# Performance work log

Measured on AMD Instinct MI355X. Metric: run time of the kernel, lower is better.

Reference implementation:

```python
import jax, jax.numpy as jnp
import numpy as np

B = 16          # graphs in batch
N = 10000       # original-graph nodes per graph
EG = 20000      # line-graph nodes (edges) per graph
E = B * EG      # total line-graph nodes
D = 384         # dim_inner
H = D // 3      # hdim
TOTAL_NODES = B * N


def setup_inputs() -> dict:
    key = jax.random.key(0)
    k1, k2 = jax.random.split(key)
    x = jax.random.normal(k1, (E, D), dtype=jnp.float32)
    org_graph_size = jnp.full((B,), N, dtype=jnp.int32)
    ptr = jnp.arange(B + 1, dtype=jnp.int32) * EG
    lg_node_idx = jax.random.randint(k2, (E, 2), 0, N, dtype=jnp.int32)
    return {"x": x, "org_graph_size": org_graph_size, "ptr": ptr, "lg_node_idx": lg_node_idx}


def _scatter_mean(x, idx, num_segments):
    # segment mean: sum / count (count clamped to 1 for empty segments)
    s = jax.ops.segment_sum(x, idx, num_segments=num_segments)
    c = jax.ops.segment_sum(jnp.ones((x.shape[0],), x.dtype), idx, num_segments=num_segments)
    return s / jnp.maximum(c, 1.0)[:, None]


def reference(x, org_graph_size, ptr, lg_node_idx):
    # per-graph node-index offsets (cumsum with leading zero, drop last)
    offsets = jnp.cumsum(
        jnp.concatenate([jnp.zeros((1,), org_graph_size.dtype), org_graph_size])
    )[:-1]
    # repeat each graph's offset for each of its line-graph nodes
    edge_counts = ptr[1:] - ptr[:-1]
    padding = jnp.repeat(offsets, edge_counts, total_repeat_length=E)
    idx = lg_node_idx + padding[:, None]  # [E, 2] global node indices

    outgoing = _scatter_mean(x, idx[:, 0], TOTAL_NODES)
    incoming = _scatter_mean(x, idx[:, 1], TOTAL_NODES)

    # lgvariant == 21
    return jnp.concatenate([incoming[:, : 2 * H], outgoing[:, 2 * H :]], axis=1)
```

## Files before the change

kernel.cpp:

```cpp
#include <hip/hip_runtime.h>

#define DIM 384
#define C4PER 96

#define SCAN_BLOCK 256
#define SCAN_ITEMS 8
#define SCAN_CHUNK (SCAN_BLOCK * SCAN_ITEMS)

__global__ void count_kernel(const int* __restrict__ org, const int* __restrict__ ptr,
                             const int2* __restrict__ lg2, int B, int E, int TN,
                             int* __restrict__ cnt, int2* __restrict__ rk) {
    int e = blockIdx.x * blockDim.x + threadIdx.x;
    if (e >= E) return;
    int off = 0;
    for (int j = 0; j < B; ++j)
        if (e >= ptr[j + 1]) off += org[j];
    int2 nn = lg2[e];
    int n_out = nn.x + off;
    int n_in  = nn.y + off;
    int r_in  = atomicAdd(&cnt[n_in], 1);
    int r_out = atomicAdd(&cnt[TN + n_out], 1);
    rk[e] = make_int2(r_out, r_in);
}

__global__ void scan1_kernel(const int* __restrict__ cnt, int* __restrict__ offs,
                             int* __restrict__ bsum, int n) {
    __shared__ int s[SCAN_BLOCK];
    int base = blockIdx.x * SCAN_CHUNK;
    int tid = threadIdx.x;
    int v[SCAN_ITEMS];
    int tsum = 0;
#pragma unroll
    for (int j = 0; j < SCAN_ITEMS; ++j) {
        int i = base + tid * SCAN_ITEMS + j;
        v[j] = (i < n) ? cnt[i] : 0;
        tsum += v[j];
    }
    s[tid] = tsum;
    __syncthreads();
    for (int d = 1; d < SCAN_BLOCK; d <<= 1) {
        int t = (tid >= d) ? s[tid - d] : 0;
        __syncthreads();
        s[tid] += t;
        __syncthreads();
    }
    if (tid == SCAN_BLOCK - 1) bsum[blockIdx.x] = s[SCAN_BLOCK - 1];
    int run = (tid > 0) ? s[tid - 1] : 0;
#pragma unroll
    for (int j = 0; j < SCAN_ITEMS; ++j) {
        int i = base + tid * SCAN_ITEMS + j;
        if (i < n) offs[i] = run;
        run += v[j];
    }
}

__global__ void scan2_kernel(int* __restrict__ bsum, int nb) {
    __shared__ int s[SCAN_BLOCK];
    int tid = threadIdx.x;
    int carry = 0;
    for (int base = 0; base < nb; base += SCAN_BLOCK) {
        int i = base + tid;
        s[tid] = (i < nb) ? bsum[i] : 0;
        __syncthreads();
        for (int d = 1; d < SCAN_BLOCK; d <<= 1) {
            int t = (tid >= d) ? s[tid - d] : 0;
            __syncthreads();
            s[tid] += t;
            __syncthreads();
        }
        int excl = carry + ((tid > 0) ? s[tid - 1] : 0);
        if (i < nb) bsum[i] = excl;
        carry += s[SCAN_BLOCK - 1];
        __syncthreads();
    }
}

__global__ void scan3_kernel(int* __restrict__ offs, const int* __restrict__ bsum, int n) {
    int i = blockIdx.x * blockDim.x + threadIdx.x;
    if (i < n) offs[i] += bsum[i / SCAN_CHUNK];
}

__global__ void fill_kernel(const int* __restrict__ org, const int* __restrict__ ptr,
                            const int2* __restrict__ lg2, const int2* __restrict__ rk,
                            const int* __restrict__ offs, int B, int E, int TN,
                            int* __restrict__ list) {
    int e = blockIdx.x * blockDim.x + threadIdx.x;
    if (e >= E) return;
    int off = 0;
    for (int j = 0; j < B; ++j)
        if (e >= ptr[j + 1]) off += org[j];
    int2 nn = lg2[e];
    int2 r  = rk[e];
    list[offs[nn.y + off] + r.y] = e;
    list[offs[TN + nn.x + off] + r.x] = e;
}

__global__ __launch_bounds__(256, 8)
void gather_kernel(const float4* __restrict__ x4,
                   const int* __restrict__ cnt, const int* __restrict__ offs,
                   const int* __restrict__ list,
                   float4* __restrict__ out4, int TN) {
    int i = blockIdx.x * blockDim.x + threadIdx.x;
    int tn64 = TN << 6;
    int node, c4, slot;
    if (i < tn64) {
        node = i >> 6;
        c4 = i & 63;
        slot = node;
    } else {
        int j = i - tn64;
        if (j >= (TN << 5)) return;
        node = j >> 5;
        c4 = 64 + (j & 31);
        slot = TN + node;
    }
    int start = offs[slot];
    int deg = cnt[slot];
    int end = start + deg;
    float4 acc = make_float4(0.f, 0.f, 0.f, 0.f);
    int k = start;
    for (; k + 1 < end; k += 2) {
        int e0 = list[k];
        int e1 = list[k + 1];
        float4 v0 = x4[e0 * C4PER + c4];
        float4 v1 = x4[e1 * C4PER + c4];
        acc.x += v0.x + v1.x;
        acc.y += v0.y + v1.y;
        acc.z += v0.z + v1.z;
        acc.w += v0.w + v1.w;
    }
    if (k < end) {
        int e0 = list[k];
        float4 v0 = x4[e0 * C4PER + c4];
        acc.x += v0.x; acc.y += v0.y; acc.z += v0.z; acc.w += v0.w;
    }
    float inv = 1.0f / (float)max(deg, 1);
    acc.x *= inv; acc.y *= inv; acc.z *= inv; acc.w *= inv;
    out4[node * C4PER + c4] = acc;
}

extern "C" void kernel_launch(void* const* d_in, const int* in_sizes, int n_in,
                              void* d_out, int out_size, void* d_ws, size_t ws_size,
                              hipStream_t stream) {
    const float* x = (const float*)d_in[0];
    const int* org = (const int*)d_in[1];
    const int* ptr = (const int*)d_in[2];
    const int* lg  = (const int*)d_in[3];

    int B  = in_sizes[1];
    int E  = in_sizes[3] / 2;
    int TN = out_size / DIM;
    int n2 = 2 * TN;

    int* cnt  = (int*)d_ws;
    int* offs = cnt + n2;
    int* bsum = offs + n2;
    int* list = bsum + 1024;
    int2* rk  = (int2*)(list + 2 * E);

    hipMemsetAsync(cnt, 0, (size_t)n2 * sizeof(int), stream);

    count_kernel<<<(E + 255) / 256, 256, 0, stream>>>(org, ptr, (const int2*)lg, B, E, TN,
                                                      cnt, rk);

    int nb = (n2 + SCAN_CHUNK - 1) / SCAN_CHUNK;
    scan1_kernel<<<nb, SCAN_BLOCK, 0, stream>>>(cnt, offs, bsum, n2);
    scan2_kernel<<<1, SCAN_BLOCK, 0, stream>>>(bsum, nb);
    scan3_kernel<<<(n2 + 255) / 256, 256, 0, stream>>>(offs, bsum, n2);

    fill_kernel<<<(E + 255) / 256, 256, 0, stream>>>(org, ptr, (const int2*)lg, rk, offs,
                                                     B, E, TN, list);

    int total = TN * C4PER;
    gather_kernel<<<(total + 255) / 256, 256, 0, stream>>>((const float4*)x, cnt, offs, list,
                                                           (float4*)d_out, TN);
}
```

Before: 759.8 us.

## Fold scan fixup into consumers, pack offset/count pairs, shuffle-broadcast edge lists

Removes the scan3 pass by having fill and gather add the block prefix (bsum[slot>>11]) on the fly. The local offset is stored together with the count as an int2, so each consumer does one load instead of two. In the gather, each lane of a wavefront (or half-wavefront) loads one list entry, and the entries are broadcast with __shfl, with a 4-way unrolled accumulation replacing serial list loads. Also adds size_t indexing and unroll pragmas, at the cost of extra shuffles and an extra bsum lookup per segment.

```diff
diff --git a/kernel.cpp b/kernel.cpp
--- a/kernel.cpp
+++ b/kernel.cpp
@@ -13,17 +13,16 @@
     int e = blockIdx.x * blockDim.x + threadIdx.x;
     if (e >= E) return;
     int off = 0;
+#pragma unroll 8
     for (int j = 0; j < B; ++j)
         if (e >= ptr[j + 1]) off += org[j];
     int2 nn = lg2[e];
-    int n_out = nn.x + off;
-    int n_in  = nn.y + off;
-    int r_in  = atomicAdd(&cnt[n_in], 1);
-    int r_out = atomicAdd(&cnt[TN + n_out], 1);
+    int r_in  = atomicAdd(&cnt[nn.y + off], 1);
+    int r_out = atomicAdd(&cnt[TN + nn.x + off], 1);
     rk[e] = make_int2(r_out, r_in);
 }
 
-__global__ void scan1_kernel(const int* __restrict__ cnt, int* __restrict__ offs,
+__global__ void scan1_kernel(const int* __restrict__ cnt, int2* __restrict__ pair,
                              int* __restrict__ bsum, int n) {
     __shared__ int s[SCAN_BLOCK];
     int base = blockIdx.x * SCAN_CHUNK;
@@ -49,7 +48,7 @@
 #pragma unroll
     for (int j = 0; j < SCAN_ITEMS; ++j) {
         int i = base + tid * SCAN_ITEMS + j;
-        if (i < n) offs[i] = run;
+        if (i < n) pair[i] = make_int2(run, v[j]);
         run += v[j];
     }
 }
@@ -75,68 +74,91 @@
     }
 }
 
-__global__ void scan3_kernel(int* __restrict__ offs, const int* __restrict__ bsum, int n) {
-    int i = blockIdx.x * blockDim.x + threadIdx.x;
-    if (i < n) offs[i] += bsum[i / SCAN_CHUNK];
-}
-
 __global__ void fill_kernel(const int* __restrict__ org, const int* __restrict__ ptr,
                             const int2* __restrict__ lg2, const int2* __restrict__ rk,
-                            const int* __restrict__ offs, int B, int E, int TN,
-                            int* __restrict__ list) {
+                            const int2* __restrict__ pair, const int* __restrict__ bsum,
+                            int B, int E, int TN, int* __restrict__ list) {
     int e = blockIdx.x * blockDim.x + threadIdx.x;
     if (e >= E) return;
     int off = 0;
+#pragma unroll 8
     for (int j = 0; j < B; ++j)
         if (e >= ptr[j + 1]) off += org[j];
     int2 nn = lg2[e];
     int2 r  = rk[e];
-    list[offs[nn.y + off] + r.y] = e;
-    list[offs[TN + nn.x + off] + r.x] = e;
+    int s_in  = nn.y + off;
+    int s_out = TN + nn.x + off;
+    list[pair[s_in].x  + bsum[s_in  >> 11] + r.y] = e;
+    list[pair[s_out].x + bsum[s_out >> 11] + r.x] = e;
+}
+
+template <int W>
+__device__ inline float4 gather_seg(const float4* __restrict__ x4,
+                                    const int* __restrict__ list,
+                                    int start, int deg, int c4, int sub) {
+    int e_l = (sub < deg) ? list[start + sub] : 0;
+    float4 acc = make_float4(0.f, 0.f, 0.f, 0.f);
+    int kf = (deg < W) ? deg : W;
+    int k = 0;
+    for (; k + 4 <= kf; k += 4) {
+        int e0 = __shfl(e_l, k,     W);
+        int e1 = __shfl(e_l, k + 1, W);
+        int e2 = __shfl(e_l, k + 2, W);
+        int e3 = __shfl(e_l, k + 3, W);
+        float4 v0 = x4[(size_t)e0 * C4PER + c4];
+        float4 v1 = x4[(size_t)e1 * C4PER + c4];
+        float4 v2 = x4[(size_t)e2 * C4PER + c4];
+        float4 v3 = x4[(size_t)e3 * C4PER + c4];
+        acc.x += (v0.x + v1.x) + (v2.x + v3.x);
+        acc.y += (v0.y + v1.y) + (v2.y + v3.y);
+        acc.z += (v0.z + v1.z) + (v2.z + v3.z);
+        acc.w += (v0.w + v1.w) + (v2.w + v3.w);
+    }
+    for (; k < kf; ++k) {
+        int e0 = __shfl(e_l, k, W);
+        float4 v = x4[(size_t)e0 * C4PER + c4];
+        acc.x += v.x; acc.y += v.y; acc.z += v.z; acc.w += v.w;
+    }
+    for (; k < deg; ++k) {
+        int e0 = list[start + k];
+        float4 v = x4[(size_t)e0 * C4PER + c4];
+        acc.x += v.x; acc.y += v.y; acc.z += v.z; acc.w += v.w;
+    }
+    return acc;
 }
 
 __global__ __launch_bounds__(256, 8)
 void gather_kernel(const float4* __restrict__ x4,
-                   const int* __restrict__ cnt, const int* __restrict__ offs,
+                   const int2* __restrict__ pair, const int* __restrict__ bsum,
                    const int* __restrict__ list,
                    float4* __restrict__ out4, int TN) {
     int i = blockIdx.x * blockDim.x + threadIdx.x;
+    int lane = threadIdx.x & 63;
     int tn64 = TN << 6;
-    int node, c4, slot;
+    float4 acc;
+    int node, c4, deg;
     if (i < tn64) {
         node = i >> 6;
         c4 = i & 63;
-        slot = node;
+        int slot = node;
+        int2 pr = pair[slot];
+        int start = pr.x + bsum[slot >> 11];
+        deg = pr.y;
+        acc = gather_seg<64>(x4, list, start, deg, c4, lane);
     } else {
         int j = i - tn64;
         if (j >= (TN << 5)) return;
         node = j >> 5;
         c4 = 64 + (j & 31);
-        slot = TN + node;
-    }
-    int start = offs[slot];
-    int deg = cnt[slot];
-    int end = start + deg;
-    float4 acc = make_float4(0.f, 0.f, 0.f, 0.f);
-    int k = start;
-    for (; k + 1 < end; k += 2) {
-        int e0 = list[k];
-        int e1 = list[k + 1];
-        float4 v0 = x4[e0 * C4PER + c4];
-        float4 v1 = x4[e1 * C4PER + c4];
-        acc.x += v0.x + v1.x;
-        acc.y += v0.y + v1.y;
-        acc.z += v0.z + v1.z;
-        acc.w += v0.w + v1.w;
-    }
-    if (k < end) {
-        int e0 = list[k];
-        float4 v0 = x4[e0 * C4PER + c4];
-        acc.x += v0.x; acc.y += v0.y; acc.z += v0.z; acc.w += v0.w;
+        int slot = TN + node;
+        int2 pr = pair[slot];
+        int start = pr.x + bsum[slot >> 11];
+        deg = pr.y;
+        acc = gather_seg<32>(x4, list, start, deg, c4, lane & 31);
     }
     float inv = 1.0f / (float)max(deg, 1);
     acc.x *= inv; acc.y *= inv; acc.z *= inv; acc.w *= inv;
-    out4[node * C4PER + c4] = acc;
+    out4[(size_t)node * C4PER + c4] = acc;
 }
 
 extern "C" void kernel_launch(void* const* d_in, const int* in_sizes, int n_in,
@@ -152,11 +174,11 @@
     int TN = out_size / DIM;
     int n2 = 2 * TN;
 
-    int* cnt  = (int*)d_ws;
-    int* offs = cnt + n2;
-    int* bsum = offs + n2;
-    int* list = bsum + 1024;
-    int2* rk  = (int2*)(list + 2 * E);
+    int* cnt   = (int*)d_ws;
+    int2* pair = (int2*)(cnt + n2);
+    int* bsum  = (int*)(pair + n2);
+    int* list  = bsum + 1024;
+    int2* rk   = (int2*)(list + 2 * E);
 
     hipMemsetAsync(cnt, 0, (size_t)n2 * sizeof(int), stream);
 
@@ -164,14 +186,13 @@
                                                       cnt, rk);
 
     int nb = (n2 + SCAN_CHUNK - 1) / SCAN_CHUNK;
-    scan1_kernel<<<nb, SCAN_BLOCK, 0, stream>>>(cnt, offs, bsum, n2);
+    scan1_kernel<<<nb, SCAN_BLOCK, 0, stream>>>(cnt, pair, bsum, n2);
     scan2_kernel<<<1, SCAN_BLOCK, 0, stream>>>(bsum, nb);
-    scan3_kernel<<<(n2 + 255) / 256, 256, 0, stream>>>(offs, bsum, n2);
 
-    fill_kernel<<<(E + 255) / 256, 256, 0, stream>>>(org, ptr, (const int2*)lg, rk, offs,
-                                                     B, E, TN, list);
+    fill_kernel<<<(E + 255) / 256, 256, 0, stream>>>(org, ptr, (const int2*)lg, rk, pair,
+                                                     bsum, B, E, TN, list);
 
     int total = TN * C4PER;
-    gather_kernel<<<(total + 255) / 256, 256, 0, stream>>>((const float4*)x, cnt, offs, list,
-                                                           (float4*)d_out, TN);
+    gather_kernel<<<(total + 255) / 256, 256, 0, stream>>>((const float4*)x, pair, bsum,
+                                                           list, (float4*)d_out, TN);
 }
```

Result: no change. 753.1 us (-0.9%).
